# Kernel optimization log

Hardware: AMD Instinct MI355X
Metric: run time of the kernel (lower is better)

The kernel has to match this reference:

```python
import jax, jax.numpy as jnp
import numpy as np

HEADS = 32
DK = 32            # att_size = hidden // heads
CUT = 15.5         # tot_dis[cur_layer=0] + 0.5
NEG = -1e8
LN_EPS = 1e-5


def layernorm(x, g, b):
    m = jnp.mean(x, axis=-1, keepdims=True)
    v = jnp.mean((x - m) ** 2, axis=-1, keepdims=True)
    return (x - m) / jnp.sqrt(v + LN_EPS) * g + b


def setup_inputs() -> dict:
    key = jax.random.key(0)
    ks = jax.random.split(key, 12)
    B, S, H, F = 8, 513, 1024, 4096
    N = S - 1
    def nrm(k, shape, scale=0.02):
        return jax.random.normal(k, shape, jnp.float32) * scale
    x = jax.random.normal(ks[0], (B, S, H), jnp.float32)
    attn_bias = jax.random.normal(ks[1], (B, HEADS, S, S), jnp.float32)
    rel_pos = jax.random.randint(ks[2], (B, N, N), 0, 16, jnp.int32)
    rel_emb = nrm(ks[3], (512, HEADS)).at[0].set(0.0)  # padding_idx=0
    Wq = nrm(ks[4], (H, H)); bq = jnp.zeros((H,), jnp.float32)
    Wk = nrm(ks[5], (H, H)); bk = jnp.zeros((H,), jnp.float32)
    Wv = nrm(ks[6], (H, H)); bv = jnp.zeros((H,), jnp.float32)
    Wo = nrm(ks[7], (H, H)); bo = jnp.zeros((H,), jnp.float32)
    W1 = nrm(ks[8], (H, F)); b1 = jnp.zeros((F,), jnp.float32)
    W2 = nrm(ks[9], (F, H)); b2 = jnp.zeros((H,), jnp.float32)
    ln1_g = jnp.ones((H,), jnp.float32); ln1_b = jnp.zeros((H,), jnp.float32)
    ln2_g = jnp.ones((H,), jnp.float32); ln2_b = jnp.zeros((H,), jnp.float32)
    return dict(x=x, attn_bias=attn_bias, rel_emb=rel_emb,
                Wq=Wq, bq=bq, Wk=Wk, bk=bk, Wv=Wv, bv=bv, Wo=Wo, bo=bo,
                W1=W1, b1=b1, W2=W2, b2=b2,
                ln1_g=ln1_g, ln1_b=ln1_b, ln2_g=ln2_g, ln2_b=ln2_b,
                rel_pos=rel_pos)


def reference(x, attn_bias, rel_emb, Wq, bq, Wk, bk, Wv, bv, Wo, bo,
              W1, b1, W2, b2, ln1_g, ln1_b, ln2_g, ln2_b, rel_pos):
    B, S, H = x.shape
    # rel-pos bias: embed [B,N,N] -> [B,N,N,heads] -> [B,heads,N,N]
    rpb = jnp.transpose(rel_emb[rel_pos], (0, 3, 1, 2))
    inner = attn_bias[:, :, 1:, 1:] + rpb
    # per-head mask flag: keep if within cutoff distance OR already -inf-masked
    flags = (rel_pos[:, None, :, :] <= CUT) | (inner < NEG)
    ab = attn_bias.at[:, :, 1:, 1:].set(inner * flags)
    # attention
    y = layernorm(x, ln1_g, ln1_b)
    scale = DK ** -0.5
    q = (y @ Wq + bq).reshape(B, S, HEADS, DK) * scale
    k = (y @ Wk + bk).reshape(B, S, HEADS, DK)
    v = (y @ Wv + bv).reshape(B, S, HEADS, DK)
    scores = jnp.einsum('bqhd,bkhd->bhqk', q, k) + ab
    attn = jax.nn.softmax(scores, axis=-1)
    o = jnp.einsum('bhqk,bkhd->bqhd', attn, v).reshape(B, S, H)
    x = x + (o @ Wo + bo)
    # FFN
    y = layernorm(x, ln2_g, ln2_b)
    y = jax.nn.gelu(y @ W1 + b1, approximate=False) @ W2 + b2
    return x + y
```

## Files before the change

kernel.cpp:

```cpp
#include <hip/hip_runtime.h>
#include <hip/hip_bf16.h>
#include <math.h>

typedef __attribute__((ext_vector_type(8))) short short8;
typedef __attribute__((ext_vector_type(4))) float f32x4;
typedef unsigned short u16;
typedef unsigned int u32;

#define SQ 513
#define MPAD 4224
#define MV 4104
#define NHEADS 32
#define DKH 32
#define SVP 576

static __device__ inline u16 f2bf(float f) {
  u32 u = __builtin_bit_cast(u32, f);
  u = (u + 0x7fffu + ((u >> 16) & 1u)) >> 16;
  return (u16)u;
}

static __device__ inline void gld16(const void* g, void* l) {
  __builtin_amdgcn_global_load_lds((__attribute__((address_space(1))) void*)g,
                                   (__attribute__((address_space(3))) void*)l,
                                   16, 0, 0);
}

static __device__ inline float gelu_f(float x) {
  return 0.5f * x * (1.f + erff(x * 0.70710678118654752f));
}

__global__ __launch_bounds__(256) void transpose_cast_k(const float* __restrict__ in,
    u16* __restrict__ out, int K, int N, float scale)
{
  __shared__ float t[32][33];
  int n0 = blockIdx.x * 32, k0 = blockIdx.y * 32;
  int tx = threadIdx.x & 31, ty = threadIdx.x >> 5;
#pragma unroll
  for (int i = 0; i < 32; i += 8)
    t[ty + i][tx] = in[(size_t)(k0 + ty + i) * N + n0 + tx];
  __syncthreads();
#pragma unroll
  for (int i = 0; i < 32; i += 8)
    out[(size_t)(n0 + ty + i) * K + k0 + tx] = f2bf(t[tx][ty + i] * scale);
}

__global__ __launch_bounds__(256) void vtrans_k(const u16* __restrict__ qkv,
    u16* __restrict__ vT)
{
  __shared__ u16 t[32][33];
  int st = blockIdx.x * 32, h = blockIdx.y, b = blockIdx.z;
  int tx = threadIdx.x & 31, ty = threadIdx.x >> 5;
#pragma unroll
  for (int i = 0; i < 32; i += 8) {
    int s = st + ty + i;
    int sc = s > 512 ? 512 : s;
    t[ty + i][tx] = qkv[(size_t)(b * SQ + sc) * 3072 + 2048 + h * DKH + tx];
  }
  __syncthreads();
#pragma unroll
  for (int i = 0; i < 32; i += 8) {
    int d = ty + i;
    vT[(((size_t)b * NHEADS + h) * DKH + d) * SVP + st + tx] = t[tx][d];
  }
}

__global__ __launch_bounds__(256) void prep_bias_k(const float* __restrict__ bq,
    const float* __restrict__ bk, const float* __restrict__ bv,
    float* __restrict__ out, float scale)
{
  int i = blockIdx.x * 256 + threadIdx.x;
  float v = (i < 1024) ? bq[i] * scale : ((i < 2048) ? bk[i - 1024] : bv[i - 2048]);
  out[i] = v;
}

__global__ __launch_bounds__(256) void ln_k(const float* __restrict__ in,
    const float* __restrict__ g, const float* __restrict__ b,
    u16* __restrict__ out)
{
  int row = blockIdx.x;
  float4 v = ((const float4*)(in + (size_t)row * 1024))[threadIdx.x];
  float s = v.x + v.y + v.z + v.w;
  float s2 = v.x * v.x + v.y * v.y + v.z * v.z + v.w * v.w;
#pragma unroll
  for (int d = 32; d; d >>= 1) { s += __shfl_xor(s, d, 64); s2 += __shfl_xor(s2, d, 64); }
  __shared__ float ps[4], ps2[4];
  int w = threadIdx.x >> 6;
  if ((threadIdx.x & 63) == 0) { ps[w] = s; ps2[w] = s2; }
  __syncthreads();
  s = ps[0] + ps[1] + ps[2] + ps[3];
  s2 = ps2[0] + ps2[1] + ps2[2] + ps2[3];
  float mean = s * (1.f / 1024.f);
  float var = s2 * (1.f / 1024.f) - mean * mean;
  float inv = rsqrtf(var + 1e-5f);
  float4 gv = ((const float4*)g)[threadIdx.x];
  float4 bv = ((const float4*)b)[threadIdx.x];
  ushort4 o;
  o.x = f2bf((v.x - mean) * inv * gv.x + bv.x);
  o.y = f2bf((v.y - mean) * inv * gv.y + bv.y);
  o.z = f2bf((v.z - mean) * inv * gv.z + bv.z);
  o.w = f2bf((v.w - mean) * inv * gv.w + bv.w);
  ((ushort4*)(out + (size_t)row * 1024))[threadIdx.x] = o;
}

template <int EPI>
__global__ __launch_bounds__(256) void gemm_bt(const u16* __restrict__ A,
    const u16* __restrict__ Bw, const float* __restrict__ bias,
    const float* __restrict__ resid, void* __restrict__ outp,
    int N, int K, int nbx)
{
  __shared__ alignas(16) u16 sA[128 * 64];
  __shared__ alignas(16) u16 sB[128 * 64];
  int tid = threadIdx.x;
  int l = tid & 63, lg = l >> 4, li = l & 15;

  int bidx = blockIdx.x;
  int kbeg = 0, kend = K;
  float* pout = (float*)outp;
  if (EPI == 4) {
    int half = gridDim.x >> 1;
    int s = bidx >= half;
    bidx -= s * half;
    kbeg = s * (K >> 1);
    kend = kbeg + (K >> 1);
    pout += (size_t)s * MPAD * 1024;
  }
  int mb = bidx / nbx, nb = bidx % nbx;
  int m0 = mb * 128, n0 = nb * 128;
  int wv = tid >> 6;
  int wr = wv >> 1, wc = wv & 1;
  f32x4 acc[4][4] = {};
  int r_ = tid >> 3, c_ = (tid & 7) * 8;
  const u16* Ag = A + (size_t)(m0 + r_) * K + c_;
  const u16* Bg = Bw + (size_t)(n0 + r_) * K + c_;
  u16* sAb = sA + (tid & 192) * 8;
  u16* sBb = sB + (tid & 192) * 8;

  for (int k0 = kbeg; k0 < kend; k0 += 64) {
    __syncthreads();
#pragma unroll
    for (int i = 0; i < 4; ++i) {
      gld16(Ag + (size_t)(i * 32) * K + k0, sAb + i * 2048);
      gld16(Bg + (size_t)(i * 32) * K + k0, sBb + i * 2048);
    }
    __syncthreads();
#pragma unroll
    for (int ks = 0; ks < 2; ++ks) {
      short8 af[4], bfr[4];
#pragma unroll
      for (int i = 0; i < 4; ++i)
        af[i] = *(const short8*)&sA[(64 * wr + 16 * i + li) * 64 + ks * 32 + lg * 8];
#pragma unroll
      for (int j = 0; j < 4; ++j)
        bfr[j] = *(const short8*)&sB[(64 * wc + 16 * j + li) * 64 + ks * 32 + lg * 8];
#pragma unroll
      for (int i = 0; i < 4; ++i)
#pragma unroll
        for (int j = 0; j < 4; ++j)
          acc[i][j] = __builtin_amdgcn_mfma_f32_16x16x32_bf16(af[i], bfr[j], acc[i][j], 0, 0, 0);
    }
  }

#pragma unroll
  for (int i = 0; i < 4; ++i) {
    int rb = m0 + 64 * wr + 16 * i + 4 * lg;
#pragma unroll
    for (int j = 0; j < 4; ++j) {
      int col = n0 + 64 * wc + 16 * j + li;
      float bia = (EPI == 4) ? 0.f : bias[col];
#pragma unroll
      for (int r = 0; r < 4; ++r) {
        int row = rb + r;
        float v = acc[i][j][r] + bia;
        if (EPI == 0) {
          ((u16*)outp)[(size_t)row * N + col] = f2bf(v);
        } else if (EPI == 1) {
          if (row < MV) {
            v += resid[(size_t)row * N + col];
            ((float*)outp)[(size_t)row * N + col] = v;
          }
        } else if (EPI == 2) {
          ((u16*)outp)[(size_t)row * N + col] = f2bf(gelu_f(v));
        } else {
          pout[(size_t)row * N + col] = v;
        }
      }
    }
  }
}

__global__ __launch_bounds__(256) void ffn2_combine(const float* __restrict__ part,
    float* __restrict__ out, const float* __restrict__ b2)
{
  size_t idx = (size_t)blockIdx.x * 256 + threadIdx.x;
  const float4* p0 = (const float4*)part;
  const float4* p1 = (const float4*)(part + (size_t)MPAD * 1024);
  float4 a = ((float4*)out)[idx];
  float4 x0 = p0[idx], x1 = p1[idx];
  float4 bb = ((const float4*)b2)[idx & 255];
  a.x += x0.x + x1.x + bb.x;
  a.y += x0.y + x1.y + bb.y;
  a.z += x0.z + x1.z + bb.z;
  a.w += x0.w + x1.w + bb.w;
  ((float4*)out)[idx] = a;
}

__global__ __launch_bounds__(256) void attn_fused(const u16* __restrict__ qkv,
    const u16* __restrict__ vT, const float* __restrict__ attn_bias,
    const int* __restrict__ rel_pos, const float* __restrict__ rel_emb,
    u16* __restrict__ o)
{
  __shared__ alignas(16) u16 k_lds[2][64 * 32];
  __shared__ alignas(16) u16 v_lds[2][32 * 64];
  __shared__ alignas(16) u16 p_lds[4][16][72];
  int bid = blockIdx.x;
  int qt = bid % 9, h = (bid / 9) % NHEADS, b = bid / (9 * NHEADS);
  int tid = threadIdx.x, wv = tid >> 6, l = tid & 63, lg = l >> 4, li = l & 15;
  int q0 = qt * 64;
  int sqb = q0 + 16 * wv + 4 * lg;

  short8 qfrag = *(const short8*)(qkv + (size_t)(b * SQ + q0 + 16 * wv + li) * 3072 + h * DKH + lg * 8);

  float tv = rel_emb[(size_t)li * NHEADS + h];

  const float* bias_row[4];
  const int* rp_row[4];
#pragma unroll
  for (int r = 0; r < 4; ++r) {
    int sq = sqb + r;
    int sqc = sq > 512 ? 512 : sq;
    bias_row[r] = attn_bias + (((size_t)b * NHEADS + h) * SQ + sqc) * SQ;
    int sqm = sq - 1; sqm = sqm < 0 ? 0 : (sqm > 511 ? 511 : sqm);
    rp_row[r] = rel_pos + ((size_t)b * 512 + sqm) * 512;
  }

  int krow = tid >> 2;
  int kchunk = (tid & 3) ^ ((tid >> 3) & 3);
  const u16* ksrc = qkv + (size_t)(b * SQ) * 3072 + 1024 + h * DKH + kchunk * 8;
  int vrow = tid >> 3;
  int vchunk = (tid & 7) ^ (vrow & 7);
  const u16* vsrc = vT + (((size_t)b * NHEADS + h) * DKH + vrow) * SVP + vchunk * 8;

  int koff[4], voff[4];
#pragma unroll
  for (int f = 0; f < 4; ++f)
    koff[f] = (16 * f + li) * 32 + ((lg ^ ((li >> 1) & 3)) * 8);
#pragma unroll
  for (int u = 0; u < 4; ++u) {
    int df = u >> 1, kk = u & 1;
    voff[u] = (16 * df + li) * 64 + (((kk * 4 + lg) ^ (li & 7)) * 8);
  }

  float pb[4][4];
  int pr[4][4];

  gld16(ksrc + (size_t)krow * 3072, (u16*)k_lds[0] + tid * 8);
  gld16(vsrc, (u16*)v_lds[0] + tid * 8);
#pragma unroll
  for (int f = 0; f < 4; ++f) {
    int sk = 16 * f + li;
    int skm = sk - 1; skm = skm < 0 ? 0 : skm;
#pragma unroll
    for (int r = 0; r < 4; ++r) {
      pb[f][r] = bias_row[r][sk];
      pr[f][r] = rp_row[r][skm];
    }
  }

  f32x4 o_acc[2] = {};
  float l_run[4] = {0.f, 0.f, 0.f, 0.f};

  for (int kt = 0; kt < 9; ++kt) {
    int cur = kt & 1;
    __syncthreads();
    if (kt < 8) {
      int s = (kt + 1) * 64 + krow; if (s > 512) s = 512;
      gld16(ksrc + (size_t)s * 3072, (u16*)k_lds[cur ^ 1] + tid * 8);
      gld16(vsrc + (size_t)(kt + 1) * 64, (u16*)v_lds[cur ^ 1] + tid * 8);
    }
    const u16* kb = k_lds[cur];
    const u16* vbf = v_lds[cur];

    f32x4 sc[4];
    __builtin_amdgcn_s_setprio(1);
#pragma unroll
    for (int f = 0; f < 4; ++f) {
      short8 kf = *(const short8*)&kb[koff[f]];
      f32x4 z = {};
      sc[f] = __builtin_amdgcn_mfma_f32_16x16x32_bf16(qfrag, kf, z, 0, 0, 0);
    }
    __builtin_amdgcn_s_setprio(0);

#pragma unroll
    for (int f = 0; f < 4; ++f) {
      int sk = kt * 64 + 16 * f + li;
#pragma unroll
      for (int r = 0; r < 4; ++r) {
        int sq = sqb + r;
        float base = pb[f][r];
        int rp = pr[f][r];
        float re = __shfl(tv, rp, 64);
        float inner = base + re;
        float ab = (rp <= 15 || inner < -1e8f) ? inner : 0.f;
        if (sq == 0 || sk == 0) ab = base;
        if (sq > 512 || sk > 512) ab = -1e30f;
        sc[f][r] += ab;
      }
    }
    if (kt < 8) {
#pragma unroll
      for (int f = 0; f < 4; ++f) {
        int sk = (kt + 1) * 64 + 16 * f + li;
        int skc = sk > 512 ? 512 : sk;
        int skm = sk - 1; skm = skm > 511 ? 511 : skm;
#pragma unroll
        for (int r = 0; r < 4; ++r) {
          pb[f][r] = bias_row[r][skc];
          pr[f][r] = rp_row[r][skm];
        }
      }
    }

#pragma unroll
    for (int f = 0; f < 4; ++f)
#pragma unroll
      for (int r = 0; r < 4; ++r) {
        float p = __expf(sc[f][r]);
        l_run[r] += p;
        p_lds[wv][4 * lg + r][16 * f + li] = f2bf(p);
      }

    __builtin_amdgcn_s_setprio(1);
#pragma unroll
    for (int kk = 0; kk < 2; ++kk) {
      short8 pa = *(const short8*)&p_lds[wv][li][kk * 32 + lg * 8];
#pragma unroll
      for (int df = 0; df < 2; ++df) {
        short8 vb = *(const short8*)&vbf[voff[df * 2 + kk]];
        o_acc[df] = __builtin_amdgcn_mfma_f32_16x16x32_bf16(pa, vb, o_acc[df], 0, 0, 0);
      }
    }
    __builtin_amdgcn_s_setprio(0);
  }

#pragma unroll
  for (int r = 0; r < 4; ++r) {
    float s = l_run[r];
#pragma unroll
    for (int d = 1; d < 16; d <<= 1) s += __shfl_xor(s, d, 16);
    l_run[r] = s;
  }
  int sqb2 = sqb;
#pragma unroll
  for (int df = 0; df < 2; ++df)
#pragma unroll
    for (int r = 0; r < 4; ++r) {
      int s_q = sqb2 + r;
      if (s_q <= 512)
        o[(size_t)(b * SQ + s_q) * 1024 + h * DKH + 16 * df + li] = f2bf(o_acc[df][r] / l_run[r]);
    }
}

extern "C" void kernel_launch(void* const* d_in, const int* in_sizes, int n_in,
                              void* d_out, int out_size, void* d_ws, size_t ws_size,
                              hipStream_t stream) {
  const float* x        = (const float*)d_in[0];
  const float* attn_bias= (const float*)d_in[1];
  const float* rel_emb  = (const float*)d_in[2];
  const float* Wq = (const float*)d_in[3];
  const float* bq = (const float*)d_in[4];
  const float* Wk = (const float*)d_in[5];
  const float* bk = (const float*)d_in[6];
  const float* Wv = (const float*)d_in[7];
  const float* bv = (const float*)d_in[8];
  const float* Wo = (const float*)d_in[9];
  const float* bo = (const float*)d_in[10];
  const float* W1 = (const float*)d_in[11];
  const float* b1 = (const float*)d_in[12];
  const float* W2 = (const float*)d_in[13];
  const float* b2 = (const float*)d_in[14];
  const float* ln1g = (const float*)d_in[15];
  const float* ln1b = (const float*)d_in[16];
  const float* ln2g = (const float*)d_in[17];
  const float* ln2b = (const float*)d_in[18];
  const int*   rel_pos = (const int*)d_in[19];
  float* out = (float*)d_out;

  char* ws = (char*)d_ws;
  size_t off = 0;
  auto alloc = [&](size_t bytes) { char* p = ws + off; off += (bytes + 255) & ~(size_t)255; return p; };
  u16* w_qkvT = (u16*)alloc((size_t)3072 * 1024 * 2);
  u16* w_oT   = (u16*)alloc((size_t)1024 * 1024 * 2);
  u16* w_1T   = (u16*)alloc((size_t)4096 * 1024 * 2);
  u16* w_2T   = (u16*)alloc((size_t)1024 * 4096 * 2);
  float* bias_qkv = (float*)alloc(3072 * 4);
  u16* ybuf = (u16*)alloc((size_t)MPAD * 1024 * 2);
  u16* obuf = (u16*)alloc((size_t)MPAD * 1024 * 2);
  u16* vTb  = (u16*)alloc((size_t)8 * NHEADS * DKH * SVP * 2);
  u16* big  = (u16*)alloc((size_t)MPAD * 4096 * 2);
  float* part = (float*)alloc((size_t)2 * MPAD * 1024 * 4);

  const float scale = 0.17677669529663689f;
  dim3 blk(256);

  transpose_cast_k<<<dim3(32, 32), blk, 0, stream>>>(Wq, w_qkvT, 1024, 1024, scale);
  transpose_cast_k<<<dim3(32, 32), blk, 0, stream>>>(Wk, w_qkvT + (size_t)1024 * 1024, 1024, 1024, 1.f);
  transpose_cast_k<<<dim3(32, 32), blk, 0, stream>>>(Wv, w_qkvT + (size_t)2048 * 1024, 1024, 1024, 1.f);
  transpose_cast_k<<<dim3(32, 32), blk, 0, stream>>>(Wo, w_oT, 1024, 1024, 1.f);
  transpose_cast_k<<<dim3(128, 32), blk, 0, stream>>>(W1, w_1T, 1024, 4096, 1.f);
  transpose_cast_k<<<dim3(32, 128), blk, 0, stream>>>(W2, w_2T, 4096, 1024, 1.f);
  prep_bias_k<<<12, blk, 0, stream>>>(bq, bk, bv, bias_qkv, scale);

  ln_k<<<MV, blk, 0, stream>>>(x, ln1g, ln1b, ybuf);
  gemm_bt<0><<<33 * 24, blk, 0, stream>>>(ybuf, w_qkvT, bias_qkv, nullptr, big, 3072, 1024, 24);
  vtrans_k<<<dim3(18, NHEADS, 8), blk, 0, stream>>>(big, vTb);
  attn_fused<<<8 * NHEADS * 9, blk, 0, stream>>>(big, vTb, attn_bias, rel_pos, rel_emb, obuf);
  gemm_bt<1><<<33 * 8, blk, 0, stream>>>(obuf, w_oT, bo, x, out, 1024, 1024, 8);
  ln_k<<<MV, blk, 0, stream>>>(out, ln2g, ln2b, ybuf);
  gemm_bt<2><<<33 * 32, blk, 0, stream>>>(ybuf, w_1T, b1, nullptr, big, 4096, 1024, 32);
  gemm_bt<4><<<33 * 8 * 2, blk, 0, stream>>>(big, w_2T, b2, nullptr, part, 1024, 4096, 8);
  ffn2_combine<<<MV, blk, 0, stream>>>(part, out, b2);
}
```

Measured before the change: 465.1 us.

## Double-buffer attention bias loads two tiles ahead with explicit vmcnt waits

The attention kernel now keeps two register sets for the bias and rel_pos values and prefetches them two key tiles ahead. The __syncthreads is replaced by an s_waitcnt vmcnt(32) plus a raw barrier, so the outstanding bias loads are not drained each iteration. Launch bounds now request 4 blocks per CU. This aims to hide global-load latency for the bias gathers, at the cost of more registers and a hand-tuned vmcnt count that must stay consistent with the number of loads in flight.

```diff
diff --git a/kernel.cpp b/kernel.cpp
--- a/kernel.cpp
+++ b/kernel.cpp
@@ -205,7 +205,7 @@
   ((float4*)out)[idx] = a;
 }
 
-__global__ __launch_bounds__(256) void attn_fused(const u16* __restrict__ qkv,
+__global__ __launch_bounds__(256, 4) void attn_fused(const u16* __restrict__ qkv,
     const u16* __restrict__ vT, const float* __restrict__ attn_bias,
     const int* __restrict__ rel_pos, const float* __restrict__ rel_emb,
     u16* __restrict__ o)
@@ -251,29 +251,37 @@
     voff[u] = (16 * df + li) * 64 + (((kk * 4 + lg) ^ (li & 7)) * 8);
   }
 
-  float pb[4][4];
-  int pr[4][4];
+  float pbA[4][4], pbB[4][4];
+  int prA[4][4], prB[4][4];
+
+  auto load_bias = [&](int kt, float (&pb)[4][4], int (&pr)[4][4]) {
+#pragma unroll
+    for (int f = 0; f < 4; ++f) {
+      int sk = kt * 64 + 16 * f + li;
+      int skc = sk > 512 ? 512 : sk;
+      int skm = sk - 1; skm = skm < 0 ? 0 : (skm > 511 ? 511 : skm);
+#pragma unroll
+      for (int r = 0; r < 4; ++r) {
+        pb[f][r] = bias_row[r][skc];
+        pr[f][r] = rp_row[r][skm];
+      }
+    }
+  };
 
   gld16(ksrc + (size_t)krow * 3072, (u16*)k_lds[0] + tid * 8);
   gld16(vsrc, (u16*)v_lds[0] + tid * 8);
-#pragma unroll
-  for (int f = 0; f < 4; ++f) {
-    int sk = 16 * f + li;
-    int skm = sk - 1; skm = skm < 0 ? 0 : skm;
-#pragma unroll
-    for (int r = 0; r < 4; ++r) {
-      pb[f][r] = bias_row[r][sk];
-      pr[f][r] = rp_row[r][skm];
-    }
-  }
+  load_bias(0, pbA, prA);
+  load_bias(1, pbB, prB);
 
   f32x4 o_acc[2] = {};
   float l_run[4] = {0.f, 0.f, 0.f, 0.f};
 
-  for (int kt = 0; kt < 9; ++kt) {
+  auto tile = [&](int kt, float (&pb)[4][4], int (&pr)[4][4], bool last) {
     int cur = kt & 1;
-    __syncthreads();
-    if (kt < 8) {
+    if (!last) asm volatile("s_waitcnt vmcnt(32)" ::: "memory");
+    else       asm volatile("s_waitcnt vmcnt(0)" ::: "memory");
+    __builtin_amdgcn_s_barrier();
+    if (!last) {
       int s = (kt + 1) * 64 + krow; if (s > 512) s = 512;
       gld16(ksrc + (size_t)s * 3072, (u16*)k_lds[cur ^ 1] + tid * 8);
       gld16(vsrc + (size_t)(kt + 1) * 64, (u16*)v_lds[cur ^ 1] + tid * 8);
@@ -307,19 +315,7 @@
         sc[f][r] += ab;
       }
     }
-    if (kt < 8) {
-#pragma unroll
-      for (int f = 0; f < 4; ++f) {
-        int sk = (kt + 1) * 64 + 16 * f + li;
-        int skc = sk > 512 ? 512 : sk;
-        int skm = sk - 1; skm = skm > 511 ? 511 : skm;
-#pragma unroll
-        for (int r = 0; r < 4; ++r) {
-          pb[f][r] = bias_row[r][skc];
-          pr[f][r] = rp_row[r][skm];
-        }
-      }
-    }
+    if (kt + 2 <= 8) load_bias(kt + 2, pb, pr);
 
 #pragma unroll
     for (int f = 0; f < 4; ++f)
@@ -341,7 +337,14 @@
       }
     }
     __builtin_amdgcn_s_setprio(0);
-  }
+  };
+
+#pragma unroll 1
+  for (int kp = 0; kp < 4; ++kp) {
+    tile(2 * kp, pbA, prA, false);
+    tile(2 * kp + 1, pbB, prB, false);
+  }
+  tile(8, pbA, prA, true);
 
 #pragma unroll
   for (int r = 0; r < 4; ++r) {
@@ -350,12 +353,11 @@
     for (int d = 1; d < 16; d <<= 1) s += __shfl_xor(s, d, 16);
     l_run[r] = s;
   }
-  int sqb2 = sqb;
 #pragma unroll
   for (int df = 0; df < 2; ++df)
 #pragma unroll
     for (int r = 0; r < 4; ++r) {
-      int s_q = sqb2 + r;
+      int s_q = sqb + r;
       if (s_q <= 512)
         o[(size_t)(b * SQ + s_q) * 1024 + h * DKH + 16 * df + li] = f2bf(o_acc[df][r] / l_run[r]);
     }
```

Result: slower. 919.2 us (+97.6%).

## Split-K the output projection and relax attention loop barrier waits

Applied to the files above, without the earlier changes.

The output projection GEMM now runs as a two-way split-K over 528 blocks instead of 264. A new combine kernel sums the two partial results and adds the bias and the residual. This is meant to fill more CUs on the small 1024x1024 GEMM, at the cost of an extra fp32 partial buffer round trip and one more launch. The attention loop replaces __syncthreads with a partial vmcnt wait plus s_barrier, adds sched_barriers, and disables unrolling, so prefetch loads can stay in flight across iterations.

```diff
diff --git a/kernel.cpp b/kernel.cpp
--- a/kernel.cpp
+++ b/kernel.cpp
@@ -174,11 +174,6 @@
         float v = acc[i][j][r] + bia;
         if (EPI == 0) {
           ((u16*)outp)[(size_t)row * N + col] = f2bf(v);
-        } else if (EPI == 1) {
-          if (row < MV) {
-            v += resid[(size_t)row * N + col];
-            ((float*)outp)[(size_t)row * N + col] = v;
-          }
         } else if (EPI == 2) {
           ((u16*)outp)[(size_t)row * N + col] = f2bf(gelu_f(v));
         } else {
@@ -187,6 +182,22 @@
       }
     }
   }
+}
+
+__global__ __launch_bounds__(256) void oproj_combine(const float* __restrict__ part,
+    float* __restrict__ out, const float* __restrict__ bo, const float* __restrict__ x)
+{
+  size_t idx = (size_t)blockIdx.x * 256 + threadIdx.x;
+  const float4* p0 = (const float4*)part;
+  const float4* p1 = (const float4*)(part + (size_t)MPAD * 1024);
+  float4 a = p0[idx], b = p1[idx];
+  float4 bb = ((const float4*)bo)[idx & 255];
+  float4 xx = ((const float4*)x)[idx];
+  a.x += b.x + bb.x + xx.x;
+  a.y += b.y + bb.y + xx.y;
+  a.z += b.z + bb.z + xx.z;
+  a.w += b.w + bb.w + xx.w;
+  ((float4*)out)[idx] = a;
 }
 
 __global__ __launch_bounds__(256) void ffn2_combine(const float* __restrict__ part,
@@ -256,6 +267,7 @@
 
   gld16(ksrc + (size_t)krow * 3072, (u16*)k_lds[0] + tid * 8);
   gld16(vsrc, (u16*)v_lds[0] + tid * 8);
+  __builtin_amdgcn_sched_barrier(0);
 #pragma unroll
   for (int f = 0; f < 4; ++f) {
     int sk = 16 * f + li;
@@ -270,14 +282,17 @@
   f32x4 o_acc[2] = {};
   float l_run[4] = {0.f, 0.f, 0.f, 0.f};
 
+#pragma unroll 1
   for (int kt = 0; kt < 9; ++kt) {
     int cur = kt & 1;
-    __syncthreads();
+    asm volatile("s_waitcnt vmcnt(32)" ::: "memory");
+    __builtin_amdgcn_s_barrier();
     if (kt < 8) {
       int s = (kt + 1) * 64 + krow; if (s > 512) s = 512;
       gld16(ksrc + (size_t)s * 3072, (u16*)k_lds[cur ^ 1] + tid * 8);
       gld16(vsrc + (size_t)(kt + 1) * 64, (u16*)v_lds[cur ^ 1] + tid * 8);
     }
+    __builtin_amdgcn_sched_barrier(0);
     const u16* kb = k_lds[cur];
     const u16* vbf = v_lds[cur];
 
@@ -350,12 +365,11 @@
     for (int d = 1; d < 16; d <<= 1) s += __shfl_xor(s, d, 16);
     l_run[r] = s;
   }
-  int sqb2 = sqb;
 #pragma unroll
   for (int df = 0; df < 2; ++df)
 #pragma unroll
     for (int r = 0; r < 4; ++r) {
-      int s_q = sqb2 + r;
+      int s_q = sqb + r;
       if (s_q <= 512)
         o[(size_t)(b * SQ + s_q) * 1024 + h * DKH + 16 * df + li] = f2bf(o_acc[df][r] / l_run[r]);
     }
@@ -415,7 +429,8 @@
   gemm_bt<0><<<33 * 24, blk, 0, stream>>>(ybuf, w_qkvT, bias_qkv, nullptr, big, 3072, 1024, 24);
   vtrans_k<<<dim3(18, NHEADS, 8), blk, 0, stream>>>(big, vTb);
   attn_fused<<<8 * NHEADS * 9, blk, 0, stream>>>(big, vTb, attn_bias, rel_pos, rel_emb, obuf);
-  gemm_bt<1><<<33 * 8, blk, 0, stream>>>(obuf, w_oT, bo, x, out, 1024, 1024, 8);
+  gemm_bt<4><<<33 * 8 * 2, blk, 0, stream>>>(obuf, w_oT, bo, nullptr, part, 1024, 1024, 8);
+  oproj_combine<<<MV, blk, 0, stream>>>(part, out, bo, x);
   ln_k<<<MV, blk, 0, stream>>>(out, ln2g, ln2b, ybuf);
   gemm_bt<2><<<33 * 32, blk, 0, stream>>>(ybuf, w_1T, b1, nullptr, big, 4096, 1024, 32);
   gemm_bt<4><<<33 * 8 * 2, blk, 0, stream>>>(big, w_2T, b2, nullptr, part, 1024, 4096, 8);
```

After: 492.0 us. +5.8%, slower.
